# Optimization experiments

Hardware: AMD Instinct MI355X
Metric: run time of the kernel (lower is better)

The kernel has to match this reference:

```python
import jax, jax.numpy as jnp
import numpy as np

N, E, G = 50000, 400000, 64
F_IN, HID, HEADS, GF, NCLS = 16, 128, 4, 10, 6


def _init(k, shape, fan):
    return jax.random.normal(k, shape, jnp.float32) * (1.0 / np.sqrt(fan))


def setup_inputs() -> dict:
    key = jax.random.key(0)
    ks = jax.random.split(key, 16)
    x = jax.random.normal(ks[0], (N, F_IN), jnp.float32)
    edge_index = jax.random.randint(ks[1], (2, E), 0, N)
    batch = jnp.sort(jax.random.randint(ks[2], (N,), 0, G))
    graph_feat = jax.random.normal(ks[3], (G, GF), jnp.float32)
    # GATConv 1: in=16 -> heads=4, out=128, concat
    W1 = _init(ks[4], (F_IN, HEADS * HID), F_IN)
    att_src1 = _init(ks[5], (HEADS, HID), HID)
    att_dst1 = _init(ks[6], (HEADS, HID), HID)
    b1 = jnp.zeros((HEADS * HID,), jnp.float32)
    # GATConv 2: in=512 -> heads=1, out=128, mean (concat=False)
    W2 = _init(ks[7], (HEADS * HID, HID), HEADS * HID)
    att_src2 = _init(ks[8], (1, HID), HID)
    att_dst2 = _init(ks[9], (1, HID), HID)
    b2 = jnp.zeros((HID,), jnp.float32)
    # graph_proj MLP 10->32->32
    Wg1 = _init(ks[10], (GF, 32), GF); bg1 = jnp.zeros((32,), jnp.float32)
    Wg2 = _init(ks[11], (32, 32), 32); bg2 = jnp.zeros((32,), jnp.float32)
    # classifier 160->128->6
    Wc1 = _init(ks[12], (HID + 32, 128), HID + 32); bc1 = jnp.zeros((128,), jnp.float32)
    Wc2 = _init(ks[13], (128, NCLS), 128); bc2 = jnp.zeros((NCLS,), jnp.float32)
    return dict(x=x, edge_index=edge_index, batch=batch, graph_feat=graph_feat,
                W1=W1, att_src1=att_src1, att_dst1=att_dst1, b1=b1,
                W2=W2, att_src2=att_src2, att_dst2=att_dst2, b2=b2,
                Wg1=Wg1, bg1=bg1, Wg2=Wg2, bg2=bg2,
                Wc1=Wc1, bc1=bc1, Wc2=Wc2, bc2=bc2)


def gat_layer(x, W, att_src, att_dst, bias, src, dst, n_nodes, heads, out_dim, concat):
    # Linear transform: [N, H, C]
    h = (x @ W).reshape(n_nodes, heads, out_dim)
    a_src = jnp.einsum('nhc,hc->nh', h, att_src)  # [N,H]
    a_dst = jnp.einsum('nhc,hc->nh', h, att_dst)  # [N,H]
    e = jax.nn.leaky_relu(a_src[src] + a_dst[dst], 0.2)  # [Etot,H]
    # segment softmax over edges grouped by dst (self-loops ensure nonempty)
    m = jax.ops.segment_max(e, dst, num_segments=n_nodes)
    ex = jnp.exp(e - m[dst])
    denom = jax.ops.segment_sum(ex, dst, num_segments=n_nodes)
    alpha = ex / denom[dst]  # [Etot,H]
    out = jax.ops.segment_sum(alpha[:, :, None] * h[src], dst, num_segments=n_nodes)  # [N,H,C]
    if concat:
        out = out.reshape(n_nodes, heads * out_dim)
    else:
        out = out.mean(axis=1)
    return out + bias


def reference(x, edge_index, batch, graph_feat,
              W1, att_src1, att_dst1, b1,
              W2, att_src2, att_dst2, b2,
              Wg1, bg1, Wg2, bg2, Wc1, bc1, Wc2, bc2):
    n = x.shape[0]
    loops = jnp.arange(n, dtype=edge_index.dtype)
    src = jnp.concatenate([edge_index[0], loops])
    dst = jnp.concatenate([edge_index[1], loops])
    h = jax.nn.elu(gat_layer(x, W1, att_src1, att_dst1, b1, src, dst, n, HEADS, HID, True))
    h = jax.nn.elu(gat_layer(h, W2, att_src2, att_dst2, b2, src, dst, n, 1, HID, False))
    # global mean pool over graphs
    g = graph_feat.shape[0]
    sums = jax.ops.segment_sum(h, batch, num_segments=g)
    counts = jax.ops.segment_sum(jnp.ones((n, 1), h.dtype), batch, num_segments=g)
    pooled = sums / jnp.maximum(counts, 1.0)
    gf = jax.nn.relu(graph_feat @ Wg1 + bg1) @ Wg2 + bg2
    z = jnp.concatenate([pooled, gf], axis=1)
    z = jax.nn.relu(z @ Wc1 + bc1)
    return z @ Wc2 + bc2
```

## Files before the change

kernel.cpp:

```cpp
#include <hip/hip_runtime.h>
#include <hip/hip_bf16.h>

#define NN 50000
#define EE 400000
#define GG 64
#define CAP 48

typedef unsigned short u16;
typedef unsigned char u8;
typedef __attribute__((ext_vector_type(8))) short bf16x8;
typedef __attribute__((ext_vector_type(4))) float f32x4;
typedef __attribute__((ext_vector_type(2))) float f32x2;

__device__ __forceinline__ float b2f(u16 u) {
    unsigned int x = ((unsigned int)u) << 16;
    return __uint_as_float(x);
}
__device__ __forceinline__ u16 f2b(float f) {
    unsigned int x = __float_as_uint(f);
    unsigned int r = x + 0x7fffu + ((x >> 16) & 1u);
    return (u16)(r >> 16);
}
__device__ __forceinline__ u8 f2fp8(float f) {
    return (u8)(__builtin_amdgcn_cvt_pk_fp8_f32(f, f, 0, false) & 0xFF);
}
__device__ __forceinline__ f32x2 fp8x2_f32(unsigned int v, bool hi) {
    return hi ? __builtin_amdgcn_cvt_pk_f32_fp8(v, true)
              : __builtin_amdgcn_cvt_pk_f32_fp8(v, false);
}
__device__ __forceinline__ float wred_sum(float v) {
    #pragma unroll
    for (int o = 32; o; o >>= 1) v += __shfl_xor(v, o, 64);
    return v;
}
__device__ __forceinline__ float lrelu(float v) { return v > 0.f ? v : 0.2f * v; }

__global__ void k_prep(const int* __restrict__ batch, int* __restrict__ deg,
                       int* __restrict__ col, int* __restrict__ gstart,
                       const float* __restrict__ W1, const float* __restrict__ as1,
                       const float* __restrict__ ad1, u16* __restrict__ W1p,
                       const float* __restrict__ W2, u16* __restrict__ W2p,
                       float* __restrict__ pooled) {
    __shared__ float asw[16][8];
    int b = blockIdx.x, t = threadIdx.x;
    if (b < 196) {
        int n = b * 256 + t;
        if (n < NN) { deg[n] = 1; col[(size_t)n * CAP] = n; }
    } else if (b == 196) {
        if (t <= GG) {
            int lo = 0, hi = NN;
            while (lo < hi) {
                int mid = (lo + hi) >> 1;
                if (batch[mid] < t) lo = mid + 1; else hi = mid;
            }
            gstart[t] = lo;
        }
    } else if (b < 453) {
        int idx = (b - 197) * 256 + t;
        int j = idx & 7;
        int l = (idx >> 3) & 63;
        int ct = idx >> 9;
        int c = ct >> 3, tt = ct & 7;
        int k = c * 32 + (l >> 4) * 8 + j;
        int n = tt * 16 + (l & 15);
        W2p[idx] = f2b(W2[k * 128 + n]);
    } else if (b == 453) {
        int pair = t >> 1, half = t & 1;
        int k = pair >> 3, h = pair & 7;
        int hd = h & 3;
        const float* att = (h >= 4) ? ad1 : as1;
        float s = 0.f;
        int c0 = half * 64;
        for (int c = c0; c < c0 + 64; c++)
            s += W1[k * 512 + hd * 128 + c] * att[hd * 128 + c];
        s += __shfl_xor(s, 1, 64);
        if (half == 0) asw[k][h] = s;
        __syncthreads();
        for (int idx = t; idx < 33 * 64 * 8; idx += 256) {
            int j = idx & 7, l = (idx >> 3) & 63, tt = idx >> 9;
            int quad = l >> 4, m = l & 15;
            int k2 = quad * 8 + j;
            float v = 0.f;
            if (k2 < 16) {
                if (tt < 32) v = W1[k2 * 512 + tt * 16 + m];
                else if (m < 8) v = asw[k2][m];
            }
            W1p[idx] = f2b(v);
        }
    } else {
        for (int i = t; i < GG * 128; i += 256) pooled[i] = 0.f;
    }
}

__global__ void k_edges(const int* __restrict__ ei, int* __restrict__ deg,
                        int* __restrict__ col) {
    int e = blockIdx.x * 256 + threadIdx.x;
    if (e < EE) {
        int s = ei[e];
        int d = ei[EE + e];
        int slot = atomicAdd(&deg[d], 1);
        if (slot < CAP) col[(size_t)d * CAP + slot] = s;
    }
}

__global__ __launch_bounds__(256) void k_gemm1(
    const float* __restrict__ x, const u16* __restrict__ W1p,
    u8* __restrict__ h1, float* __restrict__ a_src1, float* __restrict__ a_dst1) {
    int tid = threadIdx.x;
    int wave = tid >> 6, l = tid & 63;
    int quad = l >> 4, m = l & 15;
    int row0 = blockIdx.x * 64 + wave * 16;
    int arow = row0 + m;
    int arow_c = arow < NN ? arow : (NN - 1);
    bf16x8 af;
    if (quad < 2) {
        const float* xp = x + arow_c * 16 + quad * 8;
        float4 x0 = *(const float4*)(xp);
        float4 x1 = *(const float4*)(xp + 4);
        u16 tmp[8] = {f2b(x0.x), f2b(x0.y), f2b(x0.z), f2b(x0.w),
                      f2b(x1.x), f2b(x1.y), f2b(x1.z), f2b(x1.w)};
        af = *(bf16x8*)tmp;
    } else {
        af = (bf16x8){0, 0, 0, 0, 0, 0, 0, 0};
    }
    const u16* bp = W1p + l * 8;
    f32x4 acc[33];
    #pragma unroll
    for (int tt = 0; tt < 33; tt++) acc[tt] = (f32x4){0.f, 0.f, 0.f, 0.f};
    #pragma unroll
    for (int tt = 0; tt < 33; tt++) {
        bf16x8 bf = *(const bf16x8*)(bp + (size_t)tt * 512);
        acc[tt] = __builtin_amdgcn_mfma_f32_16x16x32_bf16(af, bf, acc[tt], 0, 0, 0);
    }
    #pragma unroll
    for (int r = 0; r < 4; r++) {
        int row = row0 + quad * 4 + r;
        if (row >= NN) continue;
        #pragma unroll
        for (int tt = 0; tt < 32; tt++)
            h1[(size_t)row * 512 + tt * 16 + m] = f2fp8(acc[tt][r]);
        float v = acc[32][r];
        if (m < 4) a_src1[row * 4 + m] = v;
        else if (m < 8) a_dst1[row * 4 + (m - 4)] = v;
    }
}

__global__ __launch_bounds__(256) void k_agg1(
    const int* __restrict__ deg, const int* __restrict__ col,
    const float* __restrict__ a_src1, const float* __restrict__ a_dst1,
    const u8* __restrict__ h1, const float* __restrict__ b1,
    u16* __restrict__ h2pre) {
    __shared__ float alphaS[4][CAP][4];
    int t = threadIdx.x;
    int wave = t >> 6, l = t & 63;
    int n = blockIdx.x * 4 + wave;
    if (n >= NN) return;
    int dg = min(deg[n], CAP);
    int sl = (l < dg) ? col[(size_t)n * CAP + l] : 0;
    float4 ad = *(const float4*)(a_dst1 + n * 4);
    float4 as = *(const float4*)(a_src1 + (size_t)sl * 4);
    float4 e;
    e.x = __expf(lrelu(as.x + ad.x)); e.y = __expf(lrelu(as.y + ad.y));
    e.z = __expf(lrelu(as.z + ad.z)); e.w = __expf(lrelu(as.w + ad.w));
    if (l >= dg) e = (float4){0.f, 0.f, 0.f, 0.f};
    float4 inv;
    inv.x = 1.0f / wred_sum(e.x);
    inv.y = 1.0f / wred_sum(e.y);
    inv.z = 1.0f / wred_sum(e.z);
    inv.w = 1.0f / wred_sum(e.w);
    if (l < dg) {
        float4 a4;
        a4.x = e.x * inv.x; a4.y = e.y * inv.y;
        a4.z = e.z * inv.z; a4.w = e.w * inv.w;
        *(float4*)&alphaS[wave][l][0] = a4;
    }
    int h = l >> 4;
    const u8* hb = h1 + l * 8;
    f32x2 acc[4] = {{0.f, 0.f}, {0.f, 0.f}, {0.f, 0.f}, {0.f, 0.f}};
    int iters = (dg + 1) >> 1;
    for (int j = 0; j < iters; j++) {
        int eA = 2 * j, eB = 2 * j + 1;
        int sA = __shfl(sl, eA);
        int sB = __shfl(sl, eB);
        float aA = alphaS[wave][eA][h];
        float aB = (eB < dg) ? alphaS[wave][eB][h] : 0.f;
        uint2 uA = *(const uint2*)(hb + (size_t)sA * 512);
        uint2 uB = *(const uint2*)(hb + (size_t)sB * 512);
        acc[0] += aA * fp8x2_f32(uA.x, false);
        acc[1] += aA * fp8x2_f32(uA.x, true);
        acc[2] += aA * fp8x2_f32(uA.y, false);
        acc[3] += aA * fp8x2_f32(uA.y, true);
        acc[0] += aB * fp8x2_f32(uB.x, false);
        acc[1] += aB * fp8x2_f32(uB.x, true);
        acc[2] += aB * fp8x2_f32(uB.y, false);
        acc[3] += aB * fp8x2_f32(uB.y, true);
    }
    int ch0 = l * 8;
    float4 bA = *(const float4*)(b1 + ch0);
    float4 bB = *(const float4*)(b1 + ch0 + 4);
    float av[8] = {acc[0].x, acc[0].y, acc[1].x, acc[1].y,
                   acc[2].x, acc[2].y, acc[3].x, acc[3].y};
    float bb[8] = {bA.x, bA.y, bA.z, bA.w, bB.x, bB.y, bB.z, bB.w};
    u16 ov[8];
    #pragma unroll
    for (int k = 0; k < 8; k++) {
        float v = av[k] + bb[k];
        v = v > 0.f ? v : __expf(v) - 1.0f;
        ov[k] = f2b(v);
    }
    *(bf16x8*)(h2pre + (size_t)n * 512 + ch0) = *(bf16x8*)ov;
}

__global__ __launch_bounds__(256) void k_gemm2(
    const u16* __restrict__ h2pre, const u16* __restrict__ W2p,
    const float* __restrict__ as2, const float* __restrict__ ad2,
    u8* __restrict__ hL2, float* __restrict__ a_src2, float* __restrict__ a_dst2) {
    int t = threadIdx.x;
    int wave = t >> 6, l = t & 63;
    int quad = l >> 4, m = l & 15;
    int row0 = blockIdx.x * 64 + wave * 16;
    int arow = row0 + m;
    int arow_c = arow < NN ? arow : (NN - 1);
    const u16* aptr = h2pre + (size_t)arow_c * 512 + quad * 8;
    const u16* bptr = W2p + l * 8;
    f32x4 acc[8];
    #pragma unroll
    for (int tt = 0; tt < 8; tt++) acc[tt] = (f32x4){0.f, 0.f, 0.f, 0.f};
    for (int c = 0; c < 16; c++) {
        bf16x8 af = *(const bf16x8*)(aptr + c * 32);
        #pragma unroll
        for (int tt = 0; tt < 8; tt++) {
            bf16x8 bf = *(const bf16x8*)(bptr + (size_t)(c * 8 + tt) * 512);
            acc[tt] = __builtin_amdgcn_mfma_f32_16x16x32_bf16(af, bf, acc[tt], 0, 0, 0);
        }
    }
    float asv[8], adv[8];
    #pragma unroll
    for (int tt = 0; tt < 8; tt++) {
        int colc = tt * 16 + m;
        asv[tt] = as2[colc];
        adv[tt] = ad2[colc];
    }
    #pragma unroll
    for (int r = 0; r < 4; r++) {
        int row = row0 + quad * 4 + r;
        bool ok = row < NN;
        float rs = 0.f, rd = 0.f;
        #pragma unroll
        for (int tt = 0; tt < 8; tt++) {
            float v = acc[tt][r];
            if (ok) hL2[(size_t)row * 128 + tt * 16 + m] = f2fp8(v);
            rs += v * asv[tt];
            rd += v * adv[tt];
        }
        #pragma unroll
        for (int o = 1; o < 16; o <<= 1) {
            rs += __shfl_xor(rs, o, 64);
            rd += __shfl_xor(rd, o, 64);
        }
        if (ok && m == 0) { a_src2[row] = rs; a_dst2[row] = rd; }
    }
}

__global__ __launch_bounds__(256) void k_agg2(
    const int* __restrict__ deg, const int* __restrict__ col,
    const float* __restrict__ a_src2, const float* __restrict__ a_dst2,
    const u8* __restrict__ hL2, const float* __restrict__ b2v,
    const int* __restrict__ batch, float* __restrict__ pooled) {
    __shared__ float red[4][128];
    __shared__ int gS[4];
    int t = threadIdx.x;
    int wave = t >> 6, l = t & 63;
    int n = blockIdx.x * 4 + wave;
    if (n >= NN) return;
    int dg = min(deg[n], CAP);
    int sl = (l < dg) ? col[(size_t)n * CAP + l] : 0;
    float ad = a_dst2[n];
    float e = (l < dg) ? __expf(lrelu(a_src2[sl] + ad)) : 0.f;
    float inv = 1.0f / wred_sum(e);
    float al = e * inv;
    f32x2 acc = {0.f, 0.f};
    const u8* hb = hL2 + l * 2;
    int iters = (dg + 1) >> 1;
    for (int j = 0; j < iters; j++) {
        int eA = 2 * j, eB = 2 * j + 1;
        int sA = __shfl(sl, eA);
        int sB = __shfl(sl, eB);
        float aA = __shfl(al, eA);
        float aB = __shfl(al, eB);
        unsigned int uA = *(const u16*)(hb + (size_t)sA * 128);
        unsigned int uB = *(const u16*)(hb + (size_t)sB * 128);
        acc += aA * fp8x2_f32(uA, false);
        acc += aB * fp8x2_f32(uB, false);
    }
    float o0 = acc.x + b2v[2 * l];     o0 = o0 > 0.f ? o0 : __expf(o0) - 1.0f;
    float o1 = acc.y + b2v[2 * l + 1]; o1 = o1 > 0.f ? o1 : __expf(o1) - 1.0f;
    red[wave][2 * l] = o0;
    red[wave][2 * l + 1] = o1;
    if (l == 0) gS[wave] = batch[n];
    __syncthreads();
    if (t < 128) {
        int g0 = gS[0];
        if (gS[1] == g0 && gS[2] == g0 && gS[3] == g0) {
            float s = red[0][t] + red[1][t] + red[2][t] + red[3][t];
            atomicAdd(&pooled[g0 * 128 + t], s);
        } else {
            #pragma unroll
            for (int w = 0; w < 4; w++)
                atomicAdd(&pooled[gS[w] * 128 + t], red[w][t]);
        }
    }
}

__global__ __launch_bounds__(128) void k_head(
    const int* __restrict__ gstart, const float* __restrict__ pooled,
    const float* __restrict__ gfeat,
    const float* __restrict__ Wg1, const float* __restrict__ bg1,
    const float* __restrict__ Wg2, const float* __restrict__ bg2,
    const float* __restrict__ Wc1, const float* __restrict__ bc1,
    const float* __restrict__ Wc2, const float* __restrict__ bc2,
    float* __restrict__ out) {
    __shared__ float z[160];
    __shared__ float hg[32];
    __shared__ float c1b[128];
    int g = blockIdx.x, t = threadIdx.x;
    float cntf = (float)(gstart[g + 1] - gstart[g]);
    z[t] = pooled[g * 128 + t] / fmaxf(cntf, 1.0f);
    if (t < 32) {
        float a = bg1[t];
        for (int i = 0; i < 10; i++) a += gfeat[g * 10 + i] * Wg1[i * 32 + t];
        hg[t] = fmaxf(a, 0.f);
    }
    __syncthreads();
    if (t < 32) {
        float a = bg2[t];
        for (int i = 0; i < 32; i++) a += hg[i] * Wg2[i * 32 + t];
        z[128 + t] = a;
    }
    __syncthreads();
    float a = bc1[t];
    for (int i = 0; i < 160; i++) a += z[i] * Wc1[i * 128 + t];
    c1b[t] = fmaxf(a, 0.f);
    __syncthreads();
    if (t < 6) {
        float o = bc2[t];
        for (int i = 0; i < 128; i++) o += c1b[i] * Wc2[i * 6 + t];
        out[g * 6 + t] = o;
    }
}

extern "C" void kernel_launch(void* const* d_in, const int* in_sizes, int n_in,
                              void* d_out, int out_size, void* d_ws, size_t ws_size,
                              hipStream_t stream) {
    const float* x     = (const float*)d_in[0];
    const int*   ei    = (const int*)d_in[1];
    const int*   batch = (const int*)d_in[2];
    const float* gfeat = (const float*)d_in[3];
    const float* W1    = (const float*)d_in[4];
    const float* as1   = (const float*)d_in[5];
    const float* ad1   = (const float*)d_in[6];
    const float* b1    = (const float*)d_in[7];
    const float* W2    = (const float*)d_in[8];
    const float* as2   = (const float*)d_in[9];
    const float* ad2   = (const float*)d_in[10];
    const float* b2    = (const float*)d_in[11];
    const float* Wg1   = (const float*)d_in[12];
    const float* bg1   = (const float*)d_in[13];
    const float* Wg2   = (const float*)d_in[14];
    const float* bg2   = (const float*)d_in[15];
    const float* Wc1   = (const float*)d_in[16];
    const float* bc1   = (const float*)d_in[17];
    const float* Wc2   = (const float*)d_in[18];
    const float* bc2   = (const float*)d_in[19];
    float* out = (float*)d_out;

    size_t off = 0;
    char* base = (char*)d_ws;
    auto take = [&](size_t nbytes) -> char* {
        char* p = base + off;
        off = (off + nbytes + 255) & ~(size_t)255;
        return p;
    };
    u8*    h1     = (u8*)take((size_t)NN * 512);
    u16*   h2pre  = (u16*)take((size_t)NN * 512 * 2);
    u8*    hL2    = (u8*)take((size_t)NN * 128);
    float* a_src1 = (float*)take((size_t)NN * 4 * 4);
    float* a_dst1 = (float*)take((size_t)NN * 4 * 4);
    float* a_src2 = (float*)take((size_t)NN * 4);
    float* a_dst2 = (float*)take((size_t)NN * 4);
    int*   deg    = (int*)take((size_t)NN * 4);
    int*   col    = (int*)take((size_t)NN * CAP * 4);
    float* pooled = (float*)take(GG * 128 * 4);
    int*   gstart = (int*)take((GG + 1) * 4);
    u16*   W2p    = (u16*)take((size_t)512 * 128 * 2);
    u16*   W1p    = (u16*)take((size_t)33 * 64 * 8 * 2);
    (void)ws_size; (void)in_sizes; (void)n_in; (void)out_size;

    k_prep<<<455, 256, 0, stream>>>(batch, deg, col, gstart, W1, as1, ad1, W1p,
                                    W2, W2p, pooled);
    k_edges<<<(EE + 255) / 256, 256, 0, stream>>>(ei, deg, col);
    k_gemm1<<<(NN + 63) / 64, 256, 0, stream>>>(x, W1p, h1, a_src1, a_dst1);
    k_agg1<<<(NN + 3) / 4, 256, 0, stream>>>(deg, col, a_src1, a_dst1, h1, b1, h2pre);
    k_gemm2<<<(NN + 63) / 64, 256, 0, stream>>>(h2pre, W2p, as2, ad2, hL2, a_src2, a_dst2);
    k_agg2<<<(NN + 3) / 4, 256, 0, stream>>>(deg, col, a_src2, a_dst2, hL2, b2,
                                             batch, pooled);
    k_head<<<GG, 128, 0, stream>>>(gstart, pooled, gfeat, Wg1, bg1, Wg2, bg2,
                                   Wc1, bc1, Wc2, bc2, out);
}
```

Before: 268.3 us.

## Store layer-2 input and W2 in fp8, use fp8 MFMA, unroll gathers by four

The intermediate h2pre and the packed W2 weights move from bf16 to fp8, and the second GEMM switches to the fp8 16x16x32 MFMA. This halves the write traffic in agg1 and the read traffic in gemm2. Separately, both aggregation loops now process four neighbors per iteration instead of two, giving more loads in flight. The alpha shared buffer is padded to 64 rows and written unconditionally so out-of-range lanes carry zero weight. The cost is lower precision in layer 2's input and weights.

```diff
diff --git a/kernel.cpp b/kernel.cpp
--- a/kernel.cpp
+++ b/kernel.cpp
@@ -8,6 +8,7 @@
 
 typedef unsigned short u16;
 typedef unsigned char u8;
+typedef long long i64;
 typedef __attribute__((ext_vector_type(8))) short bf16x8;
 typedef __attribute__((ext_vector_type(4))) float f32x4;
 typedef __attribute__((ext_vector_type(2))) float f32x2;
@@ -39,7 +40,7 @@
                        int* __restrict__ col, int* __restrict__ gstart,
                        const float* __restrict__ W1, const float* __restrict__ as1,
                        const float* __restrict__ ad1, u16* __restrict__ W1p,
-                       const float* __restrict__ W2, u16* __restrict__ W2p,
+                       const float* __restrict__ W2, u8* __restrict__ W2p,
                        float* __restrict__ pooled) {
     __shared__ float asw[16][8];
     int b = blockIdx.x, t = threadIdx.x;
@@ -63,7 +64,7 @@
         int c = ct >> 3, tt = ct & 7;
         int k = c * 32 + (l >> 4) * 8 + j;
         int n = tt * 16 + (l & 15);
-        W2p[idx] = f2b(W2[k * 128 + n]);
+        W2p[idx] = f2fp8(W2[k * 128 + n]);
     } else if (b == 453) {
         int pair = t >> 1, half = t & 1;
         int k = pair >> 3, h = pair & 7;
@@ -149,8 +150,8 @@
     const int* __restrict__ deg, const int* __restrict__ col,
     const float* __restrict__ a_src1, const float* __restrict__ a_dst1,
     const u8* __restrict__ h1, const float* __restrict__ b1,
-    u16* __restrict__ h2pre) {
-    __shared__ float alphaS[4][CAP][4];
+    u8* __restrict__ h2pre) {
+    __shared__ float alphaS[4][64][4];
     int t = threadIdx.x;
     int wave = t >> 6, l = t & 63;
     int n = blockIdx.x * 4 + wave;
@@ -168,7 +169,7 @@
     inv.y = 1.0f / wred_sum(e.y);
     inv.z = 1.0f / wred_sum(e.z);
     inv.w = 1.0f / wred_sum(e.w);
-    if (l < dg) {
+    {
         float4 a4;
         a4.x = e.x * inv.x; a4.y = e.y * inv.y;
         a4.z = e.z * inv.z; a4.w = e.w * inv.w;
@@ -177,23 +178,33 @@
     int h = l >> 4;
     const u8* hb = h1 + l * 8;
     f32x2 acc[4] = {{0.f, 0.f}, {0.f, 0.f}, {0.f, 0.f}, {0.f, 0.f}};
-    int iters = (dg + 1) >> 1;
+    int iters = (dg + 3) >> 2;
     for (int j = 0; j < iters; j++) {
-        int eA = 2 * j, eB = 2 * j + 1;
-        int sA = __shfl(sl, eA);
-        int sB = __shfl(sl, eB);
-        float aA = alphaS[wave][eA][h];
-        float aB = (eB < dg) ? alphaS[wave][eB][h] : 0.f;
-        uint2 uA = *(const uint2*)(hb + (size_t)sA * 512);
-        uint2 uB = *(const uint2*)(hb + (size_t)sB * 512);
-        acc[0] += aA * fp8x2_f32(uA.x, false);
-        acc[1] += aA * fp8x2_f32(uA.x, true);
-        acc[2] += aA * fp8x2_f32(uA.y, false);
-        acc[3] += aA * fp8x2_f32(uA.y, true);
-        acc[0] += aB * fp8x2_f32(uB.x, false);
-        acc[1] += aB * fp8x2_f32(uB.x, true);
-        acc[2] += aB * fp8x2_f32(uB.y, false);
-        acc[3] += aB * fp8x2_f32(uB.y, true);
+        int e0 = 4 * j, e1 = 4 * j + 1, e2 = 4 * j + 2, e3 = 4 * j + 3;
+        int s0 = __shfl(sl, e0), s1 = __shfl(sl, e1);
+        int s2 = __shfl(sl, e2), s3 = __shfl(sl, e3);
+        float a0 = alphaS[wave][e0][h], a1 = alphaS[wave][e1][h];
+        float a2 = alphaS[wave][e2][h], a3 = alphaS[wave][e3][h];
+        uint2 u0 = *(const uint2*)(hb + (size_t)s0 * 512);
+        uint2 u1 = *(const uint2*)(hb + (size_t)s1 * 512);
+        uint2 u2 = *(const uint2*)(hb + (size_t)s2 * 512);
+        uint2 u3 = *(const uint2*)(hb + (size_t)s3 * 512);
+        acc[0] += a0 * fp8x2_f32(u0.x, false);
+        acc[1] += a0 * fp8x2_f32(u0.x, true);
+        acc[2] += a0 * fp8x2_f32(u0.y, false);
+        acc[3] += a0 * fp8x2_f32(u0.y, true);
+        acc[0] += a1 * fp8x2_f32(u1.x, false);
+        acc[1] += a1 * fp8x2_f32(u1.x, true);
+        acc[2] += a1 * fp8x2_f32(u1.y, false);
+        acc[3] += a1 * fp8x2_f32(u1.y, true);
+        acc[0] += a2 * fp8x2_f32(u2.x, false);
+        acc[1] += a2 * fp8x2_f32(u2.x, true);
+        acc[2] += a2 * fp8x2_f32(u2.y, false);
+        acc[3] += a2 * fp8x2_f32(u2.y, true);
+        acc[0] += a3 * fp8x2_f32(u3.x, false);
+        acc[1] += a3 * fp8x2_f32(u3.x, true);
+        acc[2] += a3 * fp8x2_f32(u3.y, false);
+        acc[3] += a3 * fp8x2_f32(u3.y, true);
     }
     int ch0 = l * 8;
     float4 bA = *(const float4*)(b1 + ch0);
@@ -201,18 +212,22 @@
     float av[8] = {acc[0].x, acc[0].y, acc[1].x, acc[1].y,
                    acc[2].x, acc[2].y, acc[3].x, acc[3].y};
     float bb[8] = {bA.x, bA.y, bA.z, bA.w, bB.x, bB.y, bB.z, bB.w};
-    u16 ov[8];
+    float v[8];
     #pragma unroll
     for (int k = 0; k < 8; k++) {
-        float v = av[k] + bb[k];
-        v = v > 0.f ? v : __expf(v) - 1.0f;
-        ov[k] = f2b(v);
-    }
-    *(bf16x8*)(h2pre + (size_t)n * 512 + ch0) = *(bf16x8*)ov;
+        float w = av[k] + bb[k];
+        v[k] = w > 0.f ? w : __expf(w) - 1.0f;
+    }
+    unsigned int d0 = __builtin_amdgcn_cvt_pk_fp8_f32(v[0], v[1], 0, false);
+    d0 = __builtin_amdgcn_cvt_pk_fp8_f32(v[2], v[3], d0, true);
+    unsigned int d1 = __builtin_amdgcn_cvt_pk_fp8_f32(v[4], v[5], 0, false);
+    d1 = __builtin_amdgcn_cvt_pk_fp8_f32(v[6], v[7], d1, true);
+    uint2 ov; ov.x = d0; ov.y = d1;
+    *(uint2*)(h2pre + (size_t)n * 512 + ch0) = ov;
 }
 
 __global__ __launch_bounds__(256) void k_gemm2(
-    const u16* __restrict__ h2pre, const u16* __restrict__ W2p,
+    const u8* __restrict__ h2pre, const u8* __restrict__ W2p,
     const float* __restrict__ as2, const float* __restrict__ ad2,
     u8* __restrict__ hL2, float* __restrict__ a_src2, float* __restrict__ a_dst2) {
     int t = threadIdx.x;
@@ -221,17 +236,17 @@
     int row0 = blockIdx.x * 64 + wave * 16;
     int arow = row0 + m;
     int arow_c = arow < NN ? arow : (NN - 1);
-    const u16* aptr = h2pre + (size_t)arow_c * 512 + quad * 8;
-    const u16* bptr = W2p + l * 8;
+    const u8* aptr = h2pre + (size_t)arow_c * 512 + quad * 8;
+    const u8* bptr = W2p + l * 8;
     f32x4 acc[8];
     #pragma unroll
     for (int tt = 0; tt < 8; tt++) acc[tt] = (f32x4){0.f, 0.f, 0.f, 0.f};
     for (int c = 0; c < 16; c++) {
-        bf16x8 af = *(const bf16x8*)(aptr + c * 32);
+        i64 af = *(const i64*)(aptr + c * 32);
         #pragma unroll
         for (int tt = 0; tt < 8; tt++) {
-            bf16x8 bf = *(const bf16x8*)(bptr + (size_t)(c * 8 + tt) * 512);
-            acc[tt] = __builtin_amdgcn_mfma_f32_16x16x32_bf16(af, bf, acc[tt], 0, 0, 0);
+            i64 bf = *(const i64*)(bptr + (size_t)(c * 8 + tt) * 512);
+            acc[tt] = __builtin_amdgcn_mfma_f32_16x16x32_fp8_fp8(af, bf, acc[tt], 0, 0, 0);
         }
     }
     float asv[8], adv[8];
@@ -281,17 +296,21 @@
     float al = e * inv;
     f32x2 acc = {0.f, 0.f};
     const u8* hb = hL2 + l * 2;
-    int iters = (dg + 1) >> 1;
+    int iters = (dg + 3) >> 2;
     for (int j = 0; j < iters; j++) {
-        int eA = 2 * j, eB = 2 * j + 1;
-        int sA = __shfl(sl, eA);
-        int sB = __shfl(sl, eB);
-        float aA = __shfl(al, eA);
-        float aB = __shfl(al, eB);
-        unsigned int uA = *(const u16*)(hb + (size_t)sA * 128);
-        unsigned int uB = *(const u16*)(hb + (size_t)sB * 128);
-        acc += aA * fp8x2_f32(uA, false);
-        acc += aB * fp8x2_f32(uB, false);
+        int e0 = 4 * j, e1 = 4 * j + 1, e2 = 4 * j + 2, e3 = 4 * j + 3;
+        int s0 = __shfl(sl, e0), s1 = __shfl(sl, e1);
+        int s2 = __shfl(sl, e2), s3 = __shfl(sl, e3);
+        float a0 = __shfl(al, e0), a1 = __shfl(al, e1);
+        float a2 = __shfl(al, e2), a3 = __shfl(al, e3);
+        unsigned int u0 = *(const u16*)(hb + (size_t)s0 * 128);
+        unsigned int u1 = *(const u16*)(hb + (size_t)s1 * 128);
+        unsigned int u2 = *(const u16*)(hb + (size_t)s2 * 128);
+        unsigned int u3 = *(const u16*)(hb + (size_t)s3 * 128);
+        acc += a0 * fp8x2_f32(u0, false);
+        acc += a1 * fp8x2_f32(u1, false);
+        acc += a2 * fp8x2_f32(u2, false);
+        acc += a3 * fp8x2_f32(u3, false);
     }
     float o0 = acc.x + b2v[2 * l];     o0 = o0 > 0.f ? o0 : __expf(o0) - 1.0f;
     float o1 = acc.y + b2v[2 * l + 1]; o1 = o1 > 0.f ? o1 : __expf(o1) - 1.0f;
@@ -382,7 +401,7 @@
         return p;
     };
     u8*    h1     = (u8*)take((size_t)NN * 512);
-    u16*   h2pre  = (u16*)take((size_t)NN * 512 * 2);
+    u8*    h2pre  = (u8*)take((size_t)NN * 512);
     u8*    hL2    = (u8*)take((size_t)NN * 128);
     float* a_src1 = (float*)take((size_t)NN * 4 * 4);
     float* a_dst1 = (float*)take((size_t)NN * 4 * 4);
@@ -392,7 +411,7 @@
     int*   col    = (int*)take((size_t)NN * CAP * 4);
     float* pooled = (float*)take(GG * 128 * 4);
     int*   gstart = (int*)take((GG + 1) * 4);
-    u16*   W2p    = (u16*)take((size_t)512 * 128 * 2);
+    u8*    W2p    = (u8*)take((size_t)512 * 128);
     u16*   W1p    = (u16*)take((size_t)33 * 64 * 8 * 2);
     (void)ws_size; (void)in_sizes; (void)n_in; (void)out_size;
 
```

Result: faster. 256.6 us (-4.4%).
